# Kernel optimization log

Hardware: AMD Instinct MI355X
Metric: run time of the kernel (lower is better)

The kernel has to match this reference:

```python
import jax, jax.numpy as jnp
import numpy as np

DIM, HEAD_DIM, NUM_HEAD, RP_DIM = 1024, 64, 16, 256
B, N = 2, 4096
EPS_KERNEL = 1e-4


def _orthogonal_projection(nb_rows, nb_cols, rng):
    # gaussian_orthogonal_random_matrix with scaling=0 (performer-pytorch)
    blocks = []
    full = nb_rows // nb_cols
    for _ in range(full):
        q, _ = np.linalg.qr(rng.standard_normal((nb_cols, nb_cols)))
        blocks.append(q.T)
    rem = nb_rows - full * nb_cols
    if rem > 0:
        q, _ = np.linalg.qr(rng.standard_normal((nb_cols, nb_cols)))
        blocks.append(q.T[:rem])
    mat = np.concatenate(blocks, axis=0)
    multiplier = np.linalg.norm(rng.standard_normal((nb_rows, nb_cols)), axis=1)
    return (multiplier[:, None] * mat).astype(np.float32)


def setup_inputs() -> dict:
    key = jax.random.key(0)
    ks = jax.random.split(key, 10)
    s = (1.0 / np.sqrt(DIM)).astype(np.float32)
    inp = {
        'X': jax.random.normal(ks[0], (B, N, DIM), jnp.float32),
        'mask': jnp.ones((B, N), jnp.float32),
        'W_q': jax.random.normal(ks[1], (DIM, DIM), jnp.float32) * s,
        'b_q': jnp.zeros((DIM,), jnp.float32),
        'W_k': jax.random.normal(ks[2], (DIM, DIM), jnp.float32) * s,
        'b_k': jnp.zeros((DIM,), jnp.float32),
        'W_v': jax.random.normal(ks[3], (DIM, DIM), jnp.float32) * s,
        'b_v': jnp.zeros((DIM,), jnp.float32),
        'W_ff': jax.random.normal(ks[4], (DIM, DIM), jnp.float32) * s,
        'b_ff': jnp.zeros((DIM,), jnp.float32),
        'proj': jnp.asarray(_orthogonal_projection(RP_DIM, HEAD_DIM, np.random.default_rng(0))),
    }
    return inp


def _softmax_kernel(data, proj, is_query):
    # FAVOR+ positive random features (performer-pytorch softmax_kernel)
    d = data.shape[-1]
    normalizer = d ** -0.25
    ratio = proj.shape[0] ** -0.5
    data_dash = jnp.einsum('bhnd,jd->bhnj', normalizer * data, proj)
    diag_data = jnp.sum(data * data, axis=-1, keepdims=True) * 0.5 * (normalizer ** 2)
    if is_query:
        m = jnp.max(data_dash, axis=-1, keepdims=True)
    else:
        m = jnp.max(data_dash, axis=(-1, -2), keepdims=True)
    return ratio * (jnp.exp(data_dash - diag_data - m) + EPS_KERNEL)


def _split_heads(x):
    b, n, _ = x.shape
    return x.reshape(b, n, NUM_HEAD, HEAD_DIM).transpose(0, 2, 1, 3)


def reference(X, mask, W_q, b_q, W_k, b_k, W_v, b_v, W_ff, b_ff, proj):
    Q = _split_heads(X @ W_q.T + b_q)  # [B,H,N,D]
    K = _split_heads(X @ W_k.T + b_k)
    V = _split_heads(X @ W_v.T + b_v)
    scale = HEAD_DIM ** -0.25  # 1/sqrt(sqrt(head_dim)) applied in PerformerAttention.forward
    m = mask[:, None, :, None]
    qp = _softmax_kernel(Q * scale, proj, is_query=True)   # [B,H,N,R]
    kp = _softmax_kernel(K * scale * m, proj, is_query=False)
    Vm = V * m
    # non-causal linear attention
    k_sum = jnp.sum(kp, axis=-2)                                  # [B,H,R]
    D_inv = 1.0 / jnp.einsum('bhnr,bhr->bhn', qp, k_sum)          # [B,H,N]
    context = jnp.einsum('bhnr,bhne->bhre', kp, Vm)               # [B,H,R,D]
    attn = jnp.einsum('bhre,bhnr,bhn->bhne', context, qp, D_inv)  # [B,H,N,D]
    attn = attn.transpose(0, 2, 1, 3).reshape(X.shape[0], X.shape[1], NUM_HEAD * HEAD_DIM)
    return attn @ W_ff.T + b_ff
```

## Files before the change

### kernel.cpp

```cpp
#include <hip/hip_runtime.h>
#include <math.h>

typedef unsigned short u16;
typedef short bf16x8 __attribute__((ext_vector_type(8)));
typedef float f32x4 __attribute__((ext_vector_type(4)));
typedef u16 u16x4 __attribute__((ext_vector_type(4)));

#define RATIO 0.0625f
#define EPSK 1e-4f
#define LOG2E 1.44269504f

__device__ __forceinline__ float bf2f(u16 u) {
  return __uint_as_float(((unsigned)u) << 16);
}
__device__ __forceinline__ u16 f2bf(float f) {
  unsigned x = __float_as_uint(f);
  x = x + 0x7fffu + ((x >> 16) & 1u);
  return (u16)(x >> 16);
}
__device__ __forceinline__ unsigned cvtpk(float a, float b) {
  unsigned d;
  asm("v_cvt_pk_bf16_f32 %0, %1, %2" : "=v"(d) : "v"(a), "v"(b));
  return d;
}
__device__ __forceinline__ unsigned fenc(float f) {
  unsigned u = __float_as_uint(f);
  return (u & 0x80000000u) ? ~u : (u | 0x80000000u);
}
__device__ __forceinline__ float fdec(unsigned e) {
  return (e & 0x80000000u) ? __uint_as_float(e & 0x7fffffffu) : __uint_as_float(~e);
}

using as1v = __attribute__((address_space(1))) void;
using as3v = __attribute__((address_space(3))) void;
__device__ __forceinline__ void gl_lds16(const void* g, void* l) {
  __builtin_amdgcn_global_load_lds((as1v*)g, (as3v*)l, 16, 0, 0);
}

__global__ __launch_bounds__(256) void cvt_all(
    const float* __restrict__ X, const float* __restrict__ Wq, const float* __restrict__ Wk,
    const float* __restrict__ Wv, const float* __restrict__ Wff, const float* __restrict__ proj,
    u16* __restrict__ Xbf, u16* __restrict__ Wqkv, u16* __restrict__ Wffb, u16* __restrict__ Pbf) {
  long bid = blockIdx.x;
  const float* src;
  u16* dst;
  long off;
  float sc = 1.f;
  if (bid < 8192) { src = X; dst = Xbf; off = bid; }
  else if (bid < 9216) { src = Wq; dst = Wqkv; off = bid - 8192; }
  else if (bid < 10240) { src = Wk; dst = Wqkv + 1048576; off = bid - 9216; }
  else if (bid < 11264) { src = Wv; dst = Wqkv + 2097152; off = bid - 10240; }
  else if (bid < 12288) { src = Wff; dst = Wffb; off = bid - 11264; }
  else { src = proj; dst = Pbf; off = bid - 12288; sc = 0.125f; }
  long i = (off * 256 + threadIdx.x) * 4;
  f32x4 v = *(const f32x4*)(src + i);
  u16x4 o;
#pragma unroll
  for (int j = 0; j < 4; ++j) o[j] = f2bf(v[j] * sc);
  *(u16x4*)(dst + i) = o;
}

template <int EPI, int NB>
__global__ __launch_bounds__(512, 1) void gemmring(
    const u16* __restrict__ A, const u16* __restrict__ Bw,
    const float* __restrict__ bq, const float* __restrict__ bk,
    const float* __restrict__ bv, const float* __restrict__ mask,
    u16* __restrict__ Q, u16* __restrict__ Kb, u16* __restrict__ Vt,
    float* __restrict__ Of, const float* __restrict__ bff) {
  __shared__ __align__(16) u16 lds[3 * 24576];
  const int nt = 16;
  int tid = threadIdx.x;
  int l = tid & 63, w = tid >> 6;
  int wm = w >> 1, wn = w & 1;
  int lo = l & 15, hi = l >> 4;
  int bid = blockIdx.x;
  int swz = (bid & 7) * ((NB * 32) / 8) + (bid >> 3);
  long m0 = (long)(swz / NB) * 256;
  long c0 = (long)(swz % NB) * 128;
  int srow = tid >> 3;
  int sce = ((tid & 7) ^ ((tid >> 3) & 7)) * 8;
  f32x4 acc[4][4] = {};

  auto stageA = [&](int t) {
    u16* ub = (u16*)lds + (t % 3) * 24576;
    long k0 = (long)t * 64;
#pragma unroll
    for (int u = 0; u < 2; ++u)
#pragma unroll
      for (int j = 0; j < 2; ++j) {
        long row = m0 + u * 128 + j * 64 + srow;
        gl_lds16(A + row * 1024 + k0 + sce, ub + u * 8192 + j * 4096 + tid * 8);
      }
  };
  auto stageB = [&](int t) {
    u16* ub = (u16*)lds + (t % 3) * 24576 + 16384;
    long k0 = (long)t * 64;
#pragma unroll
    for (int j = 0; j < 2; ++j) {
      long row = c0 + j * 64 + srow;
      gl_lds16(Bw + row * 1024 + k0 + sce, ub + j * 4096 + tid * 8);
    }
  };

  stageA(0); stageB(0);
  stageA(1); stageB(1);

  int arb = (wm & 1) * 64;
  for (int t = 0; t < nt; ++t) {
    if (t < nt - 1) {
      asm volatile("s_waitcnt vmcnt(6)" ::: "memory");
    } else {
      asm volatile("s_waitcnt vmcnt(0)" ::: "memory");
    }
    __builtin_amdgcn_s_barrier();
    __builtin_amdgcn_sched_barrier(0);
    const u16* Au = (const u16*)lds + (t % 3) * 24576 + (wm >> 1) * 8192;
    const u16* Bu = (const u16*)lds + (t % 3) * 24576 + 16384;
    bf16x8 areg[4][2], breg[4][2];
#pragma unroll
    for (int mf = 0; mf < 4; ++mf) {
      int lrow = arb + mf * 16 + lo;
#pragma unroll
      for (int kk = 0; kk < 2; ++kk)
        areg[mf][kk] = *(const bf16x8*)(Au + lrow * 64 + ((kk * 32 + hi * 8) ^ ((lo & 7) << 3)));
    }
#pragma unroll
    for (int nf = 0; nf < 4; ++nf) {
      int lrow = wn * 64 + nf * 16 + lo;
#pragma unroll
      for (int kk = 0; kk < 2; ++kk)
        breg[nf][kk] = *(const bf16x8*)(Bu + lrow * 64 + ((kk * 32 + hi * 8) ^ ((lo & 7) << 3)));
    }
    if (t + 2 < nt) { stageA(t + 2); stageB(t + 2); }
#pragma unroll
    for (int mf = 0; mf < 4; ++mf)
#pragma unroll
      for (int nf = 0; nf < 4; ++nf)
#pragma unroll
        for (int kk = 0; kk < 2; ++kk)
          acc[mf][nf] = __builtin_amdgcn_mfma_f32_16x16x32_bf16(areg[mf][kk], breg[nf][kk],
                                                                acc[mf][nf], 0, 0, 0);
  }

  long rowb = m0 + wm * 64;
  if (EPI == 0) {
    int wsel = (int)(c0 >> 10);
    long cw = c0 & 1023;
    if (wsel < 2) {
      const float* bias = wsel ? bk : bq;
      u16* O = wsel ? Kb : Q;
#pragma unroll
      for (int mf = 0; mf < 4; ++mf)
#pragma unroll
        for (int nf = 0; nf < 4; ++nf) {
          long col = cw + wn * 64 + nf * 16 + lo;
          float bi = bias[col];
#pragma unroll
          for (int r = 0; r < 4; ++r) {
            long row = rowb + mf * 16 + hi * 4 + r;
            O[row * 1024 + col] = f2bf(acc[mf][nf][r] + bi);
          }
        }
    } else {
#pragma unroll
      for (int mf = 0; mf < 4; ++mf) {
        long t4 = rowb + mf * 16 + hi * 4;
        long b = t4 >> 12;
        long nn = t4 & 4095;
#pragma unroll
        for (int nf = 0; nf < 4; ++nf) {
          long col = cw + wn * 64 + nf * 16 + lo;
          float bi = bv[col];
          long h = col >> 6, e = col & 63;
          u16x4 pk;
#pragma unroll
          for (int r = 0; r < 4; ++r) pk[r] = f2bf((acc[mf][nf][r] + bi) * mask[t4 + r]);
          *(u16x4*)&Vt[((b * 16 + h) * 64 + e) * 4096 + nn] = pk;
        }
      }
    }
  } else {
#pragma unroll
    for (int mf = 0; mf < 4; ++mf)
#pragma unroll
      for (int nf = 0; nf < 4; ++nf) {
        long col = c0 + wn * 64 + nf * 16 + lo;
        float bi = bff[col];
#pragma unroll
        for (int r = 0; r < 4; ++r) {
          long row = rowb + mf * 16 + hi * 4 + r;
          Of[row * 1024 + col] = acc[mf][nf][r] + bi;
        }
      }
  }
}

__global__ __launch_bounds__(256) void keymax_kernel(
    const u16* __restrict__ K, const u16* __restrict__ Pbf,
    const float* __restrict__ mask, unsigned* __restrict__ menc) {
  __shared__ u16 lP[256 * 64];
  __shared__ u16 lQ[64 * 64];
  __shared__ float smask[64];
  __shared__ float swmax[4];
  int tid = threadIdx.x, l = tid & 63, w = tid >> 6;
  int h = blockIdx.y;
  long t0 = (long)blockIdx.x * 64;
  int bh = (int)(t0 >> 12) * 16 + h;
#pragma unroll
  for (int i = 0; i < 8; ++i) {
    int ch = w * 8 + i;
    gl_lds16(Pbf + (long)(ch * 8 + (l >> 3)) * 64 + (l & 7) * 8, lP + ch * 512);
  }
#pragma unroll
  for (int i = 0; i < 2; ++i) {
    int ch = w * 2 + i;
    long tok = t0 + ch * 8 + (l >> 3);
    gl_lds16(K + tok * 1024 + (long)h * 64 + (l & 7) * 8, lQ + ch * 512);
  }
  if (tid < 64) smask[tid] = mask[t0 + tid];
  asm volatile("s_waitcnt vmcnt(0)" ::: "memory");
  __syncthreads();
  f32x4 acc[4][4] = {};
  int lo = l & 15, hi = l >> 4;
#pragma unroll
  for (int k2 = 0; k2 < 2; ++k2) {
    bf16x8 af[4], bb[4];
#pragma unroll
    for (int m = 0; m < 4; ++m)
      af[m] = *(const bf16x8*)(lQ + (m * 16 + lo) * 64 + k2 * 32 + hi * 8);
#pragma unroll
    for (int n = 0; n < 4; ++n)
      bb[n] = *(const bf16x8*)(lP + (w * 64 + n * 16 + lo) * 64 + k2 * 32 + hi * 8);
#pragma unroll
    for (int m = 0; m < 4; ++m)
#pragma unroll
      for (int n = 0; n < 4; ++n)
        acc[m][n] = __builtin_amdgcn_mfma_f32_16x16x32_bf16(af[m], bb[n], acc[m][n], 0, 0, 0);
  }
  float mm = -3.4e38f;
#pragma unroll
  for (int m = 0; m < 4; ++m)
#pragma unroll
    for (int r = 0; r < 4; ++r) {
      float mv = smask[m * 16 + hi * 4 + r];
#pragma unroll
      for (int n = 0; n < 4; ++n) mm = fmaxf(mm, mv * acc[m][n][r]);
    }
#pragma unroll
  for (int s = 1; s < 64; s <<= 1) mm = fmaxf(mm, __shfl_xor(mm, s, 64));
  if (l == 0) swmax[w] = mm;
  __syncthreads();
  if (tid == 0) {
    float bm = fmaxf(fmaxf(swmax[0], swmax[1]), fmaxf(swmax[2], swmax[3]));
    atomicMax(&menc[bh], fenc(bm));
  }
}

__global__ __launch_bounds__(512) void kctx(
    const u16* __restrict__ Kg, const u16* __restrict__ Pbf,
    const u16* __restrict__ Vt, const float* __restrict__ mask,
    const unsigned* __restrict__ menc,
    float* __restrict__ part, float* __restrict__ part_ks) {
  __shared__ __align__(16) u16 projL[256 * 64];
  __shared__ __align__(16) u16 KL[256 * 64];
  __shared__ __align__(16) u16 VL[64 * 256];
  __shared__ __align__(16) u16 kpL[256 * 64];
  __shared__ float sdiag[256];
  __shared__ float smask[256];
  int tid = threadIdx.x, l = tid & 63, wq = tid >> 6;
  int lo = l & 15, hi = l >> 4;
  int bh = blockIdx.x, ck2 = blockIdx.y;
  int b = bh >> 4, h = bh & 15;
  int rq = wq * 32;
  int rl = l >> 3;
#pragma unroll
  for (int i = 0; i < 4; ++i) {
    int c = i * 8 + wq;
    int row = c * 8 + rl;
    int sc_ = ((l & 7) * 8) ^ ((row & 7) << 3);
    gl_lds16(Pbf + (long)row * 64 + sc_, projL + c * 512);
  }
  float M = fdec(menc[bh]);
  bf16x8 ones;
#pragma unroll
  for (int e = 0; e < 8; ++e) ones[e] = (short)0x3F80;
  f32x4 acc2[2][4] = {};
  f32x4 acc_ks[2] = {};
  for (int s = 0; s < 2; ++s) {
    int ck = ck2 * 2 + s;
    long tg0 = (long)b * 4096 + (long)ck * 256;
    if (s) __syncthreads();
#pragma unroll
    for (int i = 0; i < 4; ++i) {
      int c = i * 8 + wq;
      int row = c * 8 + rl;
      int sc_ = ((l & 7) * 8) ^ ((row & 7) << 3);
      gl_lds16(Kg + (tg0 + row) * 1024 + (long)h * 64 + sc_, KL + c * 512);
    }
#pragma unroll
    for (int i = 0; i < 4; ++i) {
      int c = i * 8 + wq;
      int e = 2 * c + (l >> 5);
      int sc_ = ((l & 31) * 8) ^ ((e & 7) << 3);
      gl_lds16(Vt + ((long)bh * 64 + e) * 4096 + (long)ck * 256 + sc_, VL + c * 512);
    }
    asm volatile("s_waitcnt vmcnt(0)" ::: "memory");
    __syncthreads();
    if (tid < 256) {
      float sm = 0.f;
#pragma unroll
      for (int j = 0; j < 8; ++j) {
        bf16x8 v = *(const bf16x8*)(KL + tid * 64 + ((j * 8) ^ ((tid & 7) << 3)));
#pragma unroll
        for (int e = 0; e < 8; ++e) {
          float f = bf2f((u16)v[e]);
          sm += f * f;
        }
      }
      sdiag[tid] = sm * (1.f / 128.f);
      smask[tid] = mask[tg0 + tid];
    }
    __syncthreads();
    for (int sc = 0; sc < 4; ++sc) {
      f32x4 accT[4][2] = {};
#pragma unroll
      for (int kk = 0; kk < 2; ++kk) {
        bf16x8 aK[4], bP[2];
#pragma unroll
        for (int m = 0; m < 4; ++m)
          aK[m] = *(const bf16x8*)(KL + (sc * 64 + m * 16 + lo) * 64 +
                                   ((kk * 32 + hi * 8) ^ ((lo & 7) << 3)));
#pragma unroll
        for (int nf = 0; nf < 2; ++nf)
          bP[nf] = *(const bf16x8*)(projL + (rq + nf * 16 + lo) * 64 +
                                    ((kk * 32 + hi * 8) ^ ((lo & 7) << 3)));
#pragma unroll
        for (int m = 0; m < 4; ++m)
#pragma unroll
          for (int nf = 0; nf < 2; ++nf)
            accT[m][nf] = __builtin_amdgcn_mfma_f32_16x16x32_bf16(aK[m], bP[nf], accT[m][nf], 0, 0, 0);
      }
#pragma unroll
      for (int m = 0; m < 4; ++m) {
        int tb = m * 16 + hi * 4;
        float mv[4], dg[4];
#pragma unroll
        for (int r = 0; r < 4; ++r) {
          int tk = sc * 64 + tb + r;
          mv[r] = smask[tk];
          dg[r] = sdiag[tk];
        }
#pragma unroll
        for (int nf = 0; nf < 2; ++nf) {
          int rr = rq + nf * 16 + lo;
          float v[4];
#pragma unroll
          for (int r = 0; r < 4; ++r) {
            float x = mv[r] * accT[m][nf][r] - mv[r] * mv[r] * dg[r] - M;
            v[r] = RATIO * (__builtin_exp2f(x * LOG2E) + EPSK);
          }
          uint2 pk;
          pk.x = cvtpk(v[0], v[1]);
          pk.y = cvtpk(v[2], v[3]);
          *(uint2*)(kpL + rr * 64 + (tb ^ ((lo & 7) << 3))) = pk;
        }
      }
#pragma unroll
      for (int kk = 0; kk < 2; ++kk) {
        bf16x8 aC[2], bV[4];
#pragma unroll
        for (int m = 0; m < 2; ++m)
          aC[m] = *(const bf16x8*)(kpL + (rq + m * 16 + lo) * 64 +
                                   ((kk * 32 + hi * 8) ^ ((lo & 7) << 3)));
#pragma unroll
        for (int nf = 0; nf < 4; ++nf)
          bV[nf] = *(const bf16x8*)(VL + (nf * 16 + lo) * 256 +
                                    ((sc * 64 + kk * 32 + hi * 8) ^ ((lo & 7) << 3)));
#pragma unroll
        for (int m = 0; m < 2; ++m) {
          acc_ks[m] = __builtin_amdgcn_mfma_f32_16x16x32_bf16(aC[m], ones, acc_ks[m], 0, 0, 0);
#pragma unroll
          for (int nf = 0; nf < 4; ++nf)
            acc2[m][nf] = __builtin_amdgcn_mfma_f32_16x16x32_bf16(aC[m], bV[nf], acc2[m][nf], 0, 0, 0);
        }
      }
    }
  }
  long pb = ((long)bh * 8 + ck2) * 64;
#pragma unroll
  for (int m = 0; m < 2; ++m) {
    int r0 = rq + m * 16 + hi * 4;
#pragma unroll
    for (int nf = 0; nf < 4; ++nf) {
      int e = nf * 16 + lo;
      *(f32x4*)&part[(pb + e) * 256 + r0] = acc2[m][nf];
    }
    if (lo == 0)
      *(f32x4*)&part_ks[((long)bh * 8 + ck2) * 256 + r0] = acc_ks[m];
  }
}

__global__ __launch_bounds__(256) void ctx_reduce2(const float* __restrict__ part,
                                                   const float* __restrict__ part_ks,
                                                   u16* __restrict__ ctxb) {
  int bid = blockIdx.x;
  int bh = bid / 80, j = bid % 80;
  int r = threadIdx.x;
  float s = 0.f;
  if (j < 64) {
#pragma unroll
    for (int c = 0; c < 8; ++c) s += part[(((long)bh * 8 + c) * 64 + j) * 256 + r];
  } else if (j == 64) {
#pragma unroll
    for (int c = 0; c < 8; ++c) s += part_ks[((long)bh * 8 + c) * 256 + r];
  }
  ctxb[((long)bh * 80 + j) * 256 + r] = f2bf(s);
}

__global__ __launch_bounds__(256) void qattn(
    const u16* __restrict__ Qg, const u16* __restrict__ Pbf,
    const u16* __restrict__ ctxbg, u16* __restrict__ attn) {
  __shared__ __align__(16) u16 L[69632];
  __shared__ float sdiagq[128];
  __shared__ float sredq[4 * 128];
  u16* projL = L;
  u16* CL = L + 16384;
  u16* QL = L + 36864;
  u16* qpL = L + 36864;
  int tid = threadIdx.x, l = tid & 63, wq = tid >> 6;
  int lo = l & 15, hi = l >> 4;
  int bh = blockIdx.x;
  int b = bh >> 4, h = bh & 15;
  long tokb = (long)b * 4096 + (long)blockIdx.y * 128;
  int rq = wq * 64, tq = wq * 32;
#pragma unroll
  for (int i = 0; i < 8; ++i) {
    int c = wq * 8 + i;
    int row = c * 8 + (l >> 3);
    int sc_ = ((l & 7) * 8) ^ ((row & 7) << 3);
    gl_lds16(Pbf + (long)row * 64 + sc_, projL + c * 512);
  }
#pragma unroll
  for (int i = 0; i < 4; ++i) {
    int c = wq * 4 + i;
    int row = c * 8 + (l >> 3);
    int sc_ = ((l & 7) * 8) ^ ((row & 7) << 3);
    gl_lds16(Qg + (tokb + row) * 1024 + (long)h * 64 + sc_, QL + c * 512);
  }
#pragma unroll
  for (int i = 0; i < 10; ++i) {
    int c = wq * 10 + i;
    int j = 2 * c + (l >> 5);
    int sc_ = ((l & 31) * 8) ^ ((j & 7) << 3);
    gl_lds16(ctxbg + ((long)bh * 80 + j) * 256 + sc_, CL + c * 512);
  }
  asm volatile("s_waitcnt vmcnt(0)" ::: "memory");
  __syncthreads();
  if (tid < 128) {
    float s = 0.f;
#pragma unroll
    for (int j = 0; j < 8; ++j) {
      bf16x8 v = *(const bf16x8*)(QL + tid * 64 + ((j * 8) ^ ((tid & 7) << 3)));
#pragma unroll
      for (int e = 0; e < 8; ++e) {
        float f = bf2f((u16)v[e]);
        s += f * f;
      }
    }
    sdiagq[tid] = s * (1.f / 128.f);
  }
  f32x4 acc[4][8];
#pragma unroll
  for (int m = 0; m < 4; ++m)
#pragma unroll
    for (int nf = 0; nf < 8; ++nf) acc[m][nf] = f32x4{0.f, 0.f, 0.f, 0.f};
#pragma unroll
  for (int kk = 0; kk < 2; ++kk) {
    bf16x8 aP[4], bQ[8];
#pragma unroll
    for (int m = 0; m < 4; ++m)
      aP[m] = *(const bf16x8*)(projL + (rq + m * 16 + lo) * 64 +
                               ((kk * 32 + hi * 8) ^ ((lo & 7) << 3)));
#pragma unroll
    for (int nf = 0; nf < 8; ++nf)
      bQ[nf] = *(const bf16x8*)(QL + (nf * 16 + lo) * 64 +
                                ((kk * 32 + hi * 8) ^ ((lo & 7) << 3)));
#pragma unroll
    for (int m = 0; m < 4; ++m)
#pragma unroll
      for (int nf = 0; nf < 8; ++nf)
        acc[m][nf] = __builtin_amdgcn_mfma_f32_16x16x32_bf16(aP[m], bQ[nf], acc[m][nf], 0, 0, 0);
  }
#pragma unroll
  for (int nf = 0; nf < 8; ++nf) {
    float vm = acc[0][nf][0];
#pragma unroll
    for (int m = 0; m < 4; ++m)
#pragma unroll
      for (int r = 0; r < 4; ++r) vm = fmaxf(vm, acc[m][nf][r]);
    vm = fmaxf(vm, __shfl_xor(vm, 16, 64));
    vm = fmaxf(vm, __shfl_xor(vm, 32, 64));
    if (hi == 0) sredq[wq * 128 + nf * 16 + lo] = vm;
  }
  __syncthreads();
#pragma unroll
  for (int nf = 0; nf < 8; ++nf) {
    int tk = nf * 16 + lo;
    float rm = fmaxf(fmaxf(sredq[tk], sredq[128 + tk]),
                     fmaxf(sredq[256 + tk], sredq[384 + tk]));
    float dg = sdiagq[tk];
#pragma unroll
    for (int m = 0; m < 4; ++m) {
      int r0 = rq + m * 16 + hi * 4;
      float v[4];
#pragma unroll
      for (int r = 0; r < 4; ++r) {
        float x = acc[m][nf][r] - dg - rm;
        v[r] = RATIO * (__builtin_exp2f(x * LOG2E) + EPSK);
      }
      uint2 pk;
      pk.x = cvtpk(v[0], v[1]);
      pk.y = cvtpk(v[2], v[3]);
      *(uint2*)(qpL + tk * 256 + (r0 ^ ((lo & 7) << 3))) = pk;
    }
  }
  __syncthreads();
  f32x4 acc2[5][2];
#pragma unroll
  for (int m = 0; m < 5; ++m)
#pragma unroll
    for (int n = 0; n < 2; ++n) acc2[m][n] = f32x4{0.f, 0.f, 0.f, 0.f};
#pragma unroll
  for (int ks = 0; ks < 8; ++ks) {
    bf16x8 aC[5], bQp[2];
#pragma unroll
    for (int m = 0; m < 5; ++m)
      aC[m] = *(const bf16x8*)(CL + (m * 16 + lo) * 256 +
                               ((ks * 32 + hi * 8) ^ ((lo & 7) << 3)));
#pragma unroll
    for (int n = 0; n < 2; ++n)
      bQp[n] = *(const bf16x8*)(qpL + (tq + n * 16 + lo) * 256 +
                                ((ks * 32 + hi * 8) ^ ((lo & 7) << 3)));
#pragma unroll
    for (int m = 0; m < 5; ++m)
#pragma unroll
      for (int n = 0; n < 2; ++n)
        acc2[m][n] = __builtin_amdgcn_mfma_f32_16x16x32_bf16(aC[m], bQp[n], acc2[m][n], 0, 0, 0);
  }
#pragma unroll
  for (int n = 0; n < 2; ++n) {
    float dv = __shfl(acc2[4][n][0], lo, 64);
    float di = 1.f / dv;
    long tok = tokb + tq + n * 16 + lo;
#pragma unroll
    for (int m = 0; m < 4; ++m) {
      int j0 = m * 16 + hi * 4;
      uint2 pk;
      pk.x = cvtpk(acc2[m][n][0] * di, acc2[m][n][1] * di);
      pk.y = cvtpk(acc2[m][n][2] * di, acc2[m][n][3] * di);
      *(uint2*)&attn[tok * 1024 + (long)h * 64 + j0] = pk;
    }
  }
}

extern "C" void kernel_launch(void* const* d_in, const int* in_sizes, int n_in,
                              void* d_out, int out_size, void* d_ws, size_t ws_size,
                              hipStream_t stream) {
  const float* X = (const float*)d_in[0];
  const float* mask = (const float*)d_in[1];
  const float* Wq = (const float*)d_in[2];
  const float* bq = (const float*)d_in[3];
  const float* Wk = (const float*)d_in[4];
  const float* bk = (const float*)d_in[5];
  const float* Wv = (const float*)d_in[6];
  const float* bv = (const float*)d_in[7];
  const float* Wff = (const float*)d_in[8];
  const float* bff = (const float*)d_in[9];
  const float* proj = (const float*)d_in[10];
  float* out = (float*)d_out;

  char* p = (char*)d_ws;
  u16* Xbf = (u16*)p;   p += 16777216;
  u16* Wqkv = (u16*)p;  p += 6291456;
  u16* Wffb = (u16*)p;  p += 2097152;
  u16* Pbf = (u16*)p;   p += 32768;
  u16* Qbf = (u16*)p;   p += 16777216;
  u16* Kbf = (u16*)p;   p += 16777216;
  u16* Vt = (u16*)p;    p += 16777216;
  u16* ctxb = (u16*)p;  p += 1310720;
  unsigned* menc = (unsigned*)p; p += 256;
  float* part = (float*)p;    p += 16777216;
  float* part_ks = (float*)p; p += 262144;
  u16* attn = Xbf;

  hipMemsetAsync(menc, 0, 128, stream);
  cvt_all<<<12304, 256, 0, stream>>>(X, Wq, Wk, Wv, Wff, proj, Xbf, Wqkv, Wffb, Pbf);
  gemmring<0, 24><<<768, 512, 0, stream>>>(Xbf, Wqkv, bq, bk, bv, mask, Qbf, Kbf, Vt, nullptr, nullptr);
  keymax_kernel<<<dim3(128, 16), 256, 0, stream>>>(Kbf, Pbf, mask, menc);
  kctx<<<dim3(32, 8), 512, 0, stream>>>(Kbf, Pbf, Vt, mask, menc, part, part_ks);
  ctx_reduce2<<<2560, 256, 0, stream>>>(part, part_ks, ctxb);
  qattn<<<dim3(32, 32), 256, 0, stream>>>(Qbf, Pbf, ctxb, attn);
  gemmring<1, 8><<<256, 512, 0, stream>>>(attn, Wffb, nullptr, nullptr, nullptr, nullptr,
                                          nullptr, nullptr, nullptr, out, bff);
}
```

Before: 178.0 us.

## Halve GEMM K-tile to 32 and raise occupancy hint to four blocks

The shared GEMM kernel now stages K-tiles of 32 instead of 64, which halves LDS use per block and doubles the number of pipeline iterations. The staging layout and XOR swizzle are rewritten for 64-byte rows, and the launch bound now asks for up to four 512-thread blocks per CU. The aim is more resident blocks to hide memory latency. In exchange there are twice as many barriers, fewer MFMAs between syncs, and tighter register limits that may cause spills.

```diff
diff --git a/kernel.cpp b/kernel.cpp
--- a/kernel.cpp
+++ b/kernel.cpp
@@ -61,14 +61,14 @@
 }
 
 template <int EPI, int NB>
-__global__ __launch_bounds__(512, 1) void gemmring(
+__global__ __launch_bounds__(512, 4) void gemmring(
     const u16* __restrict__ A, const u16* __restrict__ Bw,
     const float* __restrict__ bq, const float* __restrict__ bk,
     const float* __restrict__ bv, const float* __restrict__ mask,
     u16* __restrict__ Q, u16* __restrict__ Kb, u16* __restrict__ Vt,
     float* __restrict__ Of, const float* __restrict__ bff) {
-  __shared__ __align__(16) u16 lds[3 * 24576];
-  const int nt = 16;
+  __shared__ __align__(16) u16 lds[3 * 12288];
+  const int nt = 32;
   int tid = threadIdx.x;
   int l = tid & 63, w = tid >> 6;
   int wm = w >> 1, wn = w & 1;
@@ -77,69 +77,57 @@
   int swz = (bid & 7) * ((NB * 32) / 8) + (bid >> 3);
   long m0 = (long)(swz / NB) * 256;
   long c0 = (long)(swz % NB) * 128;
-  int srow = tid >> 3;
-  int sce = ((tid & 7) ^ ((tid >> 3) & 7)) * 8;
+  int srow4 = l >> 2;
+  int sce = ((l & 3) ^ ((l >> 3) & 3)) * 8;
   f32x4 acc[4][4] = {};
 
-  auto stageA = [&](int t) {
-    u16* ub = (u16*)lds + (t % 3) * 24576;
-    long k0 = (long)t * 64;
-#pragma unroll
-    for (int u = 0; u < 2; ++u)
-#pragma unroll
-      for (int j = 0; j < 2; ++j) {
-        long row = m0 + u * 128 + j * 64 + srow;
-        gl_lds16(A + row * 1024 + k0 + sce, ub + u * 8192 + j * 4096 + tid * 8);
-      }
+  auto stage = [&](int t) {
+    u16* ub = (u16*)lds + (t % 3) * 12288;
+    long k0 = (long)t * 32;
+#pragma unroll
+    for (int j = 0; j < 2; ++j) {
+      int ch = w + j * 8;
+      long row = m0 + ch * 16 + srow4;
+      gl_lds16(A + row * 1024 + k0 + sce, ub + ch * 512);
+    }
+    {
+      long row = c0 + w * 16 + srow4;
+      gl_lds16(Bw + row * 1024 + k0 + sce, ub + 8192 + w * 512);
+    }
   };
-  auto stageB = [&](int t) {
-    u16* ub = (u16*)lds + (t % 3) * 24576 + 16384;
-    long k0 = (long)t * 64;
-#pragma unroll
-    for (int j = 0; j < 2; ++j) {
-      long row = c0 + j * 64 + srow;
-      gl_lds16(Bw + row * 1024 + k0 + sce, ub + j * 4096 + tid * 8);
-    }
-  };
-
-  stageA(0); stageB(0);
-  stageA(1); stageB(1);
+
+  stage(0);
+  stage(1);
 
   int arb = (wm & 1) * 64;
   for (int t = 0; t < nt; ++t) {
     if (t < nt - 1) {
-      asm volatile("s_waitcnt vmcnt(6)" ::: "memory");
+      asm volatile("s_waitcnt vmcnt(3)" ::: "memory");
     } else {
       asm volatile("s_waitcnt vmcnt(0)" ::: "memory");
     }
     __builtin_amdgcn_s_barrier();
     __builtin_amdgcn_sched_barrier(0);
-    const u16* Au = (const u16*)lds + (t % 3) * 24576 + (wm >> 1) * 8192;
-    const u16* Bu = (const u16*)lds + (t % 3) * 24576 + 16384;
-    bf16x8 areg[4][2], breg[4][2];
+    const u16* Au = (const u16*)lds + (t % 3) * 12288 + (wm >> 1) * 4096;
+    const u16* Bu = (const u16*)lds + (t % 3) * 12288 + 8192;
+    bf16x8 areg[4], breg[4];
 #pragma unroll
     for (int mf = 0; mf < 4; ++mf) {
-      int lrow = arb + mf * 16 + lo;
-#pragma unroll
-      for (int kk = 0; kk < 2; ++kk)
-        areg[mf][kk] = *(const bf16x8*)(Au + lrow * 64 + ((kk * 32 + hi * 8) ^ ((lo & 7) << 3)));
+      int lr = arb + mf * 16 + lo;
+      areg[mf] = *(const bf16x8*)(Au + lr * 32 + ((hi * 8) ^ (((lr >> 1) & 3) << 3)));
     }
 #pragma unroll
     for (int nf = 0; nf < 4; ++nf) {
-      int lrow = wn * 64 + nf * 16 + lo;
-#pragma unroll
-      for (int kk = 0; kk < 2; ++kk)
-        breg[nf][kk] = *(const bf16x8*)(Bu + lrow * 64 + ((kk * 32 + hi * 8) ^ ((lo & 7) << 3)));
-    }
-    if (t + 2 < nt) { stageA(t + 2); stageB(t + 2); }
+      int lr = wn * 64 + nf * 16 + lo;
+      breg[nf] = *(const bf16x8*)(Bu + lr * 32 + ((hi * 8) ^ (((lr >> 1) & 3) << 3)));
+    }
+    if (t + 2 < nt) stage(t + 2);
 #pragma unroll
     for (int mf = 0; mf < 4; ++mf)
 #pragma unroll
       for (int nf = 0; nf < 4; ++nf)
-#pragma unroll
-        for (int kk = 0; kk < 2; ++kk)
-          acc[mf][nf] = __builtin_amdgcn_mfma_f32_16x16x32_bf16(areg[mf][kk], breg[nf][kk],
-                                                                acc[mf][nf], 0, 0, 0);
+        acc[mf][nf] = __builtin_amdgcn_mfma_f32_16x16x32_bf16(areg[mf], breg[nf],
+                                                              acc[mf][nf], 0, 0, 0);
   }
 
   long rowb = m0 + wm * 64;
```

Result: slower. 185.3 us (+4.1%).

## Fold global key max into kctx via online rescaling, drop keymax kernel

Applied to the files above, without the earlier changes.

Removes the separate keymax pass, which recomputed K·proj only to find the global max. kctx now keeps a per-wave running max and rescales its accumulators online, flash-style. ctx_reduce2 merges the partials with exp rescaling and adds the epsilon and ratio terms analytically, using a V column sum read from Vt. This drops one kernel launch, a memset and a full extra K-projection GEMM. In exchange it adds per-tile shuffle reductions, a rescale of the accumulators, and extra V reads in the reduce kernel. Numerics change slightly because eps is added after the bf16 rounding.

```diff
diff --git a/kernel.cpp b/kernel.cpp
--- a/kernel.cpp
+++ b/kernel.cpp
@@ -22,13 +22,6 @@
   unsigned d;
   asm("v_cvt_pk_bf16_f32 %0, %1, %2" : "=v"(d) : "v"(a), "v"(b));
   return d;
-}
-__device__ __forceinline__ unsigned fenc(float f) {
-  unsigned u = __float_as_uint(f);
-  return (u & 0x80000000u) ? ~u : (u | 0x80000000u);
-}
-__device__ __forceinline__ float fdec(unsigned e) {
-  return (e & 0x80000000u) ? __uint_as_float(e & 0x7fffffffu) : __uint_as_float(~e);
 }
 
 using as1v = __attribute__((address_space(1))) void;
@@ -195,72 +188,11 @@
   }
 }
 
-__global__ __launch_bounds__(256) void keymax_kernel(
-    const u16* __restrict__ K, const u16* __restrict__ Pbf,
-    const float* __restrict__ mask, unsigned* __restrict__ menc) {
-  __shared__ u16 lP[256 * 64];
-  __shared__ u16 lQ[64 * 64];
-  __shared__ float smask[64];
-  __shared__ float swmax[4];
-  int tid = threadIdx.x, l = tid & 63, w = tid >> 6;
-  int h = blockIdx.y;
-  long t0 = (long)blockIdx.x * 64;
-  int bh = (int)(t0 >> 12) * 16 + h;
-#pragma unroll
-  for (int i = 0; i < 8; ++i) {
-    int ch = w * 8 + i;
-    gl_lds16(Pbf + (long)(ch * 8 + (l >> 3)) * 64 + (l & 7) * 8, lP + ch * 512);
-  }
-#pragma unroll
-  for (int i = 0; i < 2; ++i) {
-    int ch = w * 2 + i;
-    long tok = t0 + ch * 8 + (l >> 3);
-    gl_lds16(K + tok * 1024 + (long)h * 64 + (l & 7) * 8, lQ + ch * 512);
-  }
-  if (tid < 64) smask[tid] = mask[t0 + tid];
-  asm volatile("s_waitcnt vmcnt(0)" ::: "memory");
-  __syncthreads();
-  f32x4 acc[4][4] = {};
-  int lo = l & 15, hi = l >> 4;
-#pragma unroll
-  for (int k2 = 0; k2 < 2; ++k2) {
-    bf16x8 af[4], bb[4];
-#pragma unroll
-    for (int m = 0; m < 4; ++m)
-      af[m] = *(const bf16x8*)(lQ + (m * 16 + lo) * 64 + k2 * 32 + hi * 8);
-#pragma unroll
-    for (int n = 0; n < 4; ++n)
-      bb[n] = *(const bf16x8*)(lP + (w * 64 + n * 16 + lo) * 64 + k2 * 32 + hi * 8);
-#pragma unroll
-    for (int m = 0; m < 4; ++m)
-#pragma unroll
-      for (int n = 0; n < 4; ++n)
-        acc[m][n] = __builtin_amdgcn_mfma_f32_16x16x32_bf16(af[m], bb[n], acc[m][n], 0, 0, 0);
-  }
-  float mm = -3.4e38f;
-#pragma unroll
-  for (int m = 0; m < 4; ++m)
-#pragma unroll
-    for (int r = 0; r < 4; ++r) {
-      float mv = smask[m * 16 + hi * 4 + r];
-#pragma unroll
-      for (int n = 0; n < 4; ++n) mm = fmaxf(mm, mv * acc[m][n][r]);
-    }
-#pragma unroll
-  for (int s = 1; s < 64; s <<= 1) mm = fmaxf(mm, __shfl_xor(mm, s, 64));
-  if (l == 0) swmax[w] = mm;
-  __syncthreads();
-  if (tid == 0) {
-    float bm = fmaxf(fmaxf(swmax[0], swmax[1]), fmaxf(swmax[2], swmax[3]));
-    atomicMax(&menc[bh], fenc(bm));
-  }
-}
-
 __global__ __launch_bounds__(512) void kctx(
     const u16* __restrict__ Kg, const u16* __restrict__ Pbf,
     const u16* __restrict__ Vt, const float* __restrict__ mask,
-    const unsigned* __restrict__ menc,
-    float* __restrict__ part, float* __restrict__ part_ks) {
+    float* __restrict__ part, float* __restrict__ part_ks,
+    float* __restrict__ part_m) {
   __shared__ __align__(16) u16 projL[256 * 64];
   __shared__ __align__(16) u16 KL[256 * 64];
   __shared__ __align__(16) u16 VL[64 * 256];
@@ -280,10 +212,10 @@
     int sc_ = ((l & 7) * 8) ^ ((row & 7) << 3);
     gl_lds16(Pbf + (long)row * 64 + sc_, projL + c * 512);
   }
-  float M = fdec(menc[bh]);
   bf16x8 ones;
 #pragma unroll
   for (int e = 0; e < 8; ++e) ones[e] = (short)0x3F80;
+  float Mw = -3.4e38f;
   f32x4 acc2[2][4] = {};
   f32x4 acc_ks[2] = {};
   for (int s = 0; s < 2; ++s) {
@@ -340,6 +272,30 @@
           for (int nf = 0; nf < 2; ++nf)
             accT[m][nf] = __builtin_amdgcn_mfma_f32_16x16x32_bf16(aK[m], bP[nf], accT[m][nf], 0, 0, 0);
       }
+      float mloc = -3.4e38f;
+#pragma unroll
+      for (int m = 0; m < 4; ++m) {
+        int tb = m * 16 + hi * 4;
+#pragma unroll
+        for (int r = 0; r < 4; ++r) {
+          float mv = smask[sc * 64 + tb + r];
+#pragma unroll
+          for (int nf = 0; nf < 2; ++nf) mloc = fmaxf(mloc, mv * accT[m][nf][r]);
+        }
+      }
+#pragma unroll
+      for (int sft = 1; sft < 64; sft <<= 1) mloc = fmaxf(mloc, __shfl_xor(mloc, sft, 64));
+      float nM = fmaxf(Mw, mloc);
+      float rs = __builtin_exp2f((Mw - nM) * LOG2E);
+#pragma unroll
+      for (int m = 0; m < 2; ++m)
+#pragma unroll
+        for (int q = 0; q < 4; ++q) {
+          acc_ks[m][q] *= rs;
+#pragma unroll
+          for (int nf = 0; nf < 4; ++nf) acc2[m][nf][q] *= rs;
+        }
+      Mw = nM;
 #pragma unroll
       for (int m = 0; m < 4; ++m) {
         int tb = m * 16 + hi * 4;
@@ -356,8 +312,8 @@
           float v[4];
 #pragma unroll
           for (int r = 0; r < 4; ++r) {
-            float x = mv[r] * accT[m][nf][r] - mv[r] * mv[r] * dg[r] - M;
-            v[r] = RATIO * (__builtin_exp2f(x * LOG2E) + EPSK);
+            float x = mv[r] * accT[m][nf][r] - mv[r] * mv[r] * dg[r] - Mw;
+            v[r] = __builtin_exp2f(x * LOG2E);
           }
           uint2 pk;
           pk.x = cvtpk(v[0], v[1]);
@@ -398,23 +354,59 @@
     if (lo == 0)
       *(f32x4*)&part_ks[((long)bh * 8 + ck2) * 256 + r0] = acc_ks[m];
   }
-}
-
-__global__ __launch_bounds__(256) void ctx_reduce2(const float* __restrict__ part,
-                                                   const float* __restrict__ part_ks,
-                                                   u16* __restrict__ ctxb) {
+  if (l == 0) part_m[((long)bh * 8 + ck2) * 8 + wq] = Mw;
+}
+
+__global__ __launch_bounds__(256) void ctx_reduce2(
+    const float* __restrict__ part, const float* __restrict__ part_ks,
+    const float* __restrict__ part_m, const u16* __restrict__ Vt,
+    u16* __restrict__ ctxb) {
+  __shared__ float red[256];
   int bid = blockIdx.x;
   int bh = bid / 80, j = bid % 80;
   int r = threadIdx.x;
-  float s = 0.f;
+  const float* pm = part_m + (long)bh * 64;
+  float M = -3.4e38f;
+#pragma unroll
+  for (int i = 0; i < 64; ++i) M = fmaxf(M, pm[i]);
+  int wv = r >> 5;
+  float out = 0.f;
   if (j < 64) {
-#pragma unroll
-    for (int c = 0; c < 8; ++c) s += part[(((long)bh * 8 + c) * 64 + j) * 256 + r];
+    float s = 0.f;
+#pragma unroll
+    for (int c = 0; c < 8; ++c)
+      s += __builtin_exp2f((pm[c * 8 + wv] - M) * LOG2E) *
+           part[(((long)bh * 8 + c) * 64 + j) * 256 + r];
+    float sv = 0.f;
+    const u16* vr = Vt + ((long)bh * 64 + j) * 4096 + r * 16;
+#pragma unroll
+    for (int q = 0; q < 2; ++q) {
+      bf16x8 v = *(const bf16x8*)(vr + q * 8);
+#pragma unroll
+      for (int e = 0; e < 8; ++e) sv += bf2f((u16)v[e]);
+    }
+    red[r] = sv;
+    __syncthreads();
+    if (r < 32) {
+      float t = 0.f;
+#pragma unroll
+      for (int i = 0; i < 8; ++i) t += red[r * 8 + i];
+      red[r] = t;
+    }
+    __syncthreads();
+    float svt = 0.f;
+#pragma unroll
+    for (int i = 0; i < 32; ++i) svt += red[i];
+    out = RATIO * (s + EPSK * svt);
   } else if (j == 64) {
-#pragma unroll
-    for (int c = 0; c < 8; ++c) s += part_ks[((long)bh * 8 + c) * 256 + r];
-  }
-  ctxb[((long)bh * 80 + j) * 256 + r] = f2bf(s);
+    float s = 0.f;
+#pragma unroll
+    for (int c = 0; c < 8; ++c)
+      s += __builtin_exp2f((pm[c * 8 + wv] - M) * LOG2E) *
+           part_ks[((long)bh * 8 + c) * 256 + r];
+    out = RATIO * (s + EPSK * 4096.f);
+  }
+  ctxb[((long)bh * 80 + j) * 256 + r] = f2bf(out);
 }
 
 __global__ __launch_bounds__(256) void qattn(
@@ -588,17 +580,15 @@
   u16* Kbf = (u16*)p;   p += 16777216;
   u16* Vt = (u16*)p;    p += 16777216;
   u16* ctxb = (u16*)p;  p += 1310720;
-  unsigned* menc = (unsigned*)p; p += 256;
   float* part = (float*)p;    p += 16777216;
   float* part_ks = (float*)p; p += 262144;
+  float* part_m = (float*)p;  p += 8192;
   u16* attn = Xbf;
 
-  hipMemsetAsync(menc, 0, 128, stream);
   cvt_all<<<12304, 256, 0, stream>>>(X, Wq, Wk, Wv, Wff, proj, Xbf, Wqkv, Wffb, Pbf);
   gemmring<0, 24><<<768, 512, 0, stream>>>(Xbf, Wqkv, bq, bk, bv, mask, Qbf, Kbf, Vt, nullptr, nullptr);
-  keymax_kernel<<<dim3(128, 16), 256, 0, stream>>>(Kbf, Pbf, mask, menc);
-  kctx<<<dim3(32, 8), 512, 0, stream>>>(Kbf, Pbf, Vt, mask, menc, part, part_ks);
-  ctx_reduce2<<<2560, 256, 0, stream>>>(part, part_ks, ctxb);
+  kctx<<<dim3(32, 8), 512, 0, stream>>>(Kbf, Pbf, Vt, mask, part, part_ks, part_m);
+  ctx_reduce2<<<2560, 256, 0, stream>>>(part, part_ks, part_m, Vt, ctxb);
   qattn<<<dim3(32, 32), 256, 0, stream>>>(Qbf, Pbf, ctxb, attn);
   gemmring<1, 8><<<256, 512, 0, stream>>>(attn, Wffb, nullptr, nullptr, nullptr, nullptr,
                                           nullptr, nullptr, nullptr, out, bff);
```

After: 162.3 us. 1.1x faster.
